# Kernel optimization log

Measured on AMD Instinct MI355X. Metric: run time of the kernel, lower is better.

## Reference

```python
import jax, jax.numpy as jnp
import numpy as np

BS = 16384
NUM_CLASSES = 8192


def setup_inputs() -> dict:
    key = jax.random.key(0)
    k1, k2 = jax.random.split(key)
    output = jax.random.normal(k1, (BS, NUM_CLASSES), dtype=jnp.float32)
    target = jax.random.randint(k2, (BS,), 0, NUM_CLASSES, dtype=jnp.int64)
    return {"output": output, "target": target}


def reference(output, target):
    # mode == 'train' branch of SelfFilterLoss, fully vectorized.
    bs, num_classes = output.shape
    log_prob = jax.nn.log_softmax(output, axis=1)          # [bs, C]
    # standard cross entropy (mean reduction)
    tgt = target[:, None]
    loss_ce = -jnp.mean(jnp.take_along_axis(log_prob, tgt, axis=1))
    # pseudo labels = softmax(output)
    pseudo_label = jnp.exp(log_prob)                        # [bs, C]
    # per-row confidence at the (noisy) target class
    max_ = jnp.take_along_axis(pseudo_label, tgt, axis=1)   # [bs, 1]
    confident = 0.2 - pseudo_label / max_                   # [bs, C]
    latent_labels = jnp.where(confident >= 0.0, confident, 0.0)
    # one_lossF: -sum(log_softmax * one_hot) / bs
    one_loss = -jnp.sum(log_prob * latent_labels) / bs
    conf_penalty = 0.1 * one_loss / (num_classes - 1)
    return loss_ce + conf_penalty
```

## Files before the change

kernel.cpp:

```cpp
#include <hip/hip_runtime.h>
#include <math.h>

constexpr int BS = 16384;
constexpr int NC = 8192;
constexpr int THREADS = 256;
constexpr int V4PT = NC / (THREADS * 4);

using nt4 = __attribute__((ext_vector_type(4))) float;

__launch_bounds__(THREADS)
__global__ void self_filter_row_kernel(const float* __restrict__ x,
                                       const int* __restrict__ tgt,
                                       float* __restrict__ partial) {
    const int row  = blockIdx.x;
    const int t    = threadIdx.x;
    const int wave = t >> 6;
    const int lane = t & 63;

    const nt4* rowp = reinterpret_cast<const nt4*>(x + (size_t)row * NC);
    const int tr = tgt[row];

    __shared__ float s_xt;
    __shared__ float s_m[4];
    __shared__ float s_se[4], s_xl[4], s_l[4];

    nt4 v[V4PT];
#pragma unroll
    for (int i = 0; i < V4PT; ++i) {
        const int idx4 = i * THREADS + t;
        v[i] = __builtin_nontemporal_load(&rowp[idx4]);
        const int base = idx4 * 4;
        const int d = tr - base;
        if (d >= 0 && d < 4) {
            s_xt = v[i][tr & 3];
        }
    }

    float m = -INFINITY;
#pragma unroll
    for (int i = 0; i < V4PT; ++i)
        m = fmaxf(m, fmaxf(fmaxf(v[i][0], v[i][1]), fmaxf(v[i][2], v[i][3])));
#pragma unroll
    for (int off = 32; off > 0; off >>= 1)
        m = fmaxf(m, __shfl_xor(m, off, 64));
    if (lane == 0) s_m[wave] = m;
    __syncthreads();
    m = fmaxf(fmaxf(s_m[0], s_m[1]), fmaxf(s_m[2], s_m[3]));
    const float xt = s_xt;
    const float K  = __expf(m - xt);

    float sum_e = 0.0f, sum_xl = 0.0f, sum_l = 0.0f;
#pragma unroll
    for (int i = 0; i < V4PT; ++i) {
#pragma unroll
        for (int k = 0; k < 4; ++k) {
            const float xv  = v[i][k];
            const float ex  = __expf(xv - m);
            sum_e += ex;
            const float conf = 0.2f - ex * K;
            const float lat  = conf > 0.0f ? conf : 0.0f;
            sum_xl = fmaf(xv, lat, sum_xl);
            sum_l += lat;
        }
    }

#pragma unroll
    for (int off = 32; off > 0; off >>= 1) {
        sum_e  += __shfl_xor(sum_e,  off, 64);
        sum_xl += __shfl_xor(sum_xl, off, 64);
        sum_l  += __shfl_xor(sum_l,  off, 64);
    }
    if (lane == 0) { s_se[wave] = sum_e; s_xl[wave] = sum_xl; s_l[wave] = sum_l; }
    __syncthreads();

    if (t == 0) {
        const float S   = s_se[0] + s_se[1] + s_se[2] + s_se[3];
        const float XL  = s_xl[0] + s_xl[1] + s_xl[2] + s_xl[3];
        const float L   = s_l[0]  + s_l[1]  + s_l[2]  + s_l[3];
        const float lse = __logf(S);
        const float off_ = m + lse;
        const float total = XL - off_ * L;
        const float lp_t  = xt - off_;
        partial[row] = -lp_t - (0.1f / (float)(NC - 1)) * total;
    }
}

__launch_bounds__(THREADS)
__global__ void self_filter_reduce_kernel(const float* __restrict__ partial,
                                          float* __restrict__ out) {
    const int t    = threadIdx.x;
    const int wave = t >> 6;
    const int lane = t & 63;
    __shared__ float s_s[4];

    const nt4* p4 = reinterpret_cast<const nt4*>(partial);
    float s = 0.0f;
#pragma unroll
    for (int i = 0; i < BS / (THREADS * 4); ++i) {
        const nt4 v = p4[i * THREADS + t];
        s += (v[0] + v[1]) + (v[2] + v[3]);
    }
#pragma unroll
    for (int off = 32; off > 0; off >>= 1)
        s += __shfl_xor(s, off, 64);
    if (lane == 0) s_s[wave] = s;
    __syncthreads();
    if (t == 0)
        out[0] = (s_s[0] + s_s[1] + s_s[2] + s_s[3]) * (1.0f / (float)BS);
}

extern "C" void kernel_launch(void* const* d_in, const int* in_sizes, int n_in,
                              void* d_out, int out_size, void* d_ws, size_t ws_size,
                              hipStream_t stream) {
    const float* x   = (const float*)d_in[0];
    const int*   tgt = (const int*)d_in[1];
    float*       out = (float*)d_out;
    float*       partial = (float*)d_ws;

    self_filter_row_kernel<<<BS, THREADS, 0, stream>>>(x, tgt, partial);
    self_filter_reduce_kernel<<<1, THREADS, 0, stream>>>(partial, out);
}
```

Before: 639.2 us.

## Replace block-wide max barrier with per-thread online softmax merge using exp2

After: 672.9 us. 1.05x slower.

```diff
diff --git a/kernel.cpp b/kernel.cpp
--- a/kernel.cpp
+++ b/kernel.cpp
@@ -6,7 +6,7 @@
 constexpr int THREADS = 256;
 constexpr int V4PT = NC / (THREADS * 4);
 
-using nt4 = __attribute__((ext_vector_type(4))) float;
+using f4 = __attribute__((ext_vector_type(4))) float;
 
 __launch_bounds__(THREADS)
 __global__ void self_filter_row_kernel(const float* __restrict__ x,
@@ -17,69 +17,68 @@
     const int wave = t >> 6;
     const int lane = t & 63;
 
-    const nt4* rowp = reinterpret_cast<const nt4*>(x + (size_t)row * NC);
-    const int tr = tgt[row];
+    const f4* rowp = reinterpret_cast<const f4*>(x + (size_t)row * NC);
+    const int   tr = tgt[row];
+    const float xt = x[(size_t)row * NC + tr];
 
-    __shared__ float s_xt;
-    __shared__ float s_m[4];
-    __shared__ float s_se[4], s_xl[4], s_l[4];
+    __shared__ float s_my[4], s_se[4], s_xl[4], s_l[4];
 
-    nt4 v[V4PT];
-#pragma unroll
-    for (int i = 0; i < V4PT; ++i) {
-        const int idx4 = i * THREADS + t;
-        v[i] = __builtin_nontemporal_load(&rowp[idx4]);
-        const int base = idx4 * 4;
-        const int d = tr - base;
-        if (d >= 0 && d < 4) {
-            s_xt = v[i][tr & 3];
-        }
-    }
-
-    float m = -INFINITY;
+    f4 v[V4PT];
 #pragma unroll
     for (int i = 0; i < V4PT; ++i)
-        m = fmaxf(m, fmaxf(fmaxf(v[i][0], v[i][1]), fmaxf(v[i][2], v[i][3])));
+        v[i] = rowp[i * THREADS + t];
+
+    float mx = -INFINITY;
 #pragma unroll
-    for (int off = 32; off > 0; off >>= 1)
-        m = fmaxf(m, __shfl_xor(m, off, 64));
-    if (lane == 0) s_m[wave] = m;
-    __syncthreads();
-    m = fmaxf(fmaxf(s_m[0], s_m[1]), fmaxf(s_m[2], s_m[3]));
-    const float xt = s_xt;
-    const float K  = __expf(m - xt);
+    for (int i = 0; i < V4PT; ++i)
+        mx = fmaxf(mx, fmaxf(fmaxf(v[i][0], v[i][1]), fmaxf(v[i][2], v[i][3])));
 
-    float sum_e = 0.0f, sum_xl = 0.0f, sum_l = 0.0f;
+    const float L  = 1.4426950408889634f;
+    float my = mx * L;
+    const float yt = xt * L;
+
+    float se = 0.0f, sxl = 0.0f, sl = 0.0f;
 #pragma unroll
     for (int i = 0; i < V4PT; ++i) {
 #pragma unroll
         for (int k = 0; k < 4; ++k) {
-            const float xv  = v[i][k];
-            const float ex  = __expf(xv - m);
-            sum_e += ex;
-            const float conf = 0.2f - ex * K;
+            const float xv = v[i][k];
+            const float y  = xv * L;
+            se += __builtin_amdgcn_exp2f(y - my);
+            const float e2 = __builtin_amdgcn_exp2f(y - yt);
+            const float conf = 0.2f - e2;
             const float lat  = conf > 0.0f ? conf : 0.0f;
-            sum_xl = fmaf(xv, lat, sum_xl);
-            sum_l += lat;
+            sxl = fmaf(xv, lat, sxl);
+            sl += lat;
         }
     }
 
 #pragma unroll
     for (int off = 32; off > 0; off >>= 1) {
-        sum_e  += __shfl_xor(sum_e,  off, 64);
-        sum_xl += __shfl_xor(sum_xl, off, 64);
-        sum_l  += __shfl_xor(sum_l,  off, 64);
+        const float my2 = __shfl_xor(my, off, 64);
+        const float se2 = __shfl_xor(se, off, 64);
+        const float mn  = fmaxf(my, my2);
+        se = se  * __builtin_amdgcn_exp2f(my  - mn)
+           + se2 * __builtin_amdgcn_exp2f(my2 - mn);
+        my = mn;
+        sxl += __shfl_xor(sxl, off, 64);
+        sl  += __shfl_xor(sl,  off, 64);
     }
-    if (lane == 0) { s_se[wave] = sum_e; s_xl[wave] = sum_xl; s_l[wave] = sum_l; }
+    if (lane == 0) { s_my[wave] = my; s_se[wave] = se; s_xl[wave] = sxl; s_l[wave] = sl; }
     __syncthreads();
 
     if (t == 0) {
-        const float S   = s_se[0] + s_se[1] + s_se[2] + s_se[3];
-        const float XL  = s_xl[0] + s_xl[1] + s_xl[2] + s_xl[3];
-        const float L   = s_l[0]  + s_l[1]  + s_l[2]  + s_l[3];
-        const float lse = __logf(S);
-        const float off_ = m + lse;
-        const float total = XL - off_ * L;
+        const float M = fmaxf(fmaxf(s_my[0], s_my[1]), fmaxf(s_my[2], s_my[3]));
+        float S = 0.0f, XL = 0.0f, SL = 0.0f;
+#pragma unroll
+        for (int w = 0; w < 4; ++w) {
+            S  += s_se[w] * __builtin_amdgcn_exp2f(s_my[w] - M);
+            XL += s_xl[w];
+            SL += s_l[w];
+        }
+        const float LN2 = 0.69314718055994531f;
+        const float off_  = LN2 * (M + __builtin_amdgcn_logf(S));
+        const float total = XL - off_ * SL;
         const float lp_t  = xt - off_;
         partial[row] = -lp_t - (0.1f / (float)(NC - 1)) * total;
     }
@@ -93,11 +92,11 @@
     const int lane = t & 63;
     __shared__ float s_s[4];
 
-    const nt4* p4 = reinterpret_cast<const nt4*>(partial);
+    const f4* p4 = reinterpret_cast<const f4*>(partial);
     float s = 0.0f;
 #pragma unroll
     for (int i = 0; i < BS / (THREADS * 4); ++i) {
-        const nt4 v = p4[i * THREADS + t];
+        const f4 v = p4[i * THREADS + t];
         s += (v[0] + v[1]) + (v[2] + v[3]);
     }
 #pragma unroll
```
